# Optimization experiments

Measured on AMD Instinct MI355X. Metric: run time of the kernel, lower is better.

The kernel has to match this reference:

```python
import jax, jax.numpy as jnp
from jax import lax
import numpy as np

B, C, H, W = 64, 3, 224, 224
NPARAM, NSEV, NCHROMA, K = 8, 5, 1, 37
SEVERITY = 3  # ctor default
CHROMA = 0   # random.random()*nchroma made deterministic


def setup_inputs() -> dict:
    key = jax.random.key(0)
    k1, k2, k3, k4, k5 = jax.random.split(key, 5)
    batch = jax.random.uniform(k1, (B, C, H, W), dtype=jnp.float32)
    targets = jax.random.randint(k2, (B,), 0, 1000, dtype=jnp.int32)
    psf_stack = jax.random.uniform(k3, (NPARAM, NSEV, NCHROMA, C, K, K), dtype=jnp.float32)
    params = jax.random.randint(k4, (B,), 0, NPARAM, dtype=jnp.int32)
    weights = jax.random.uniform(k5, (B,), dtype=jnp.float32)
    return {"batch": batch, "targets": targets, "psf_stack": psf_stack,
            "params": params, "weights": weights}


def reference(batch, targets, psf_stack, params, weights):
    # kernels for chosen severity/chroma: [NPARAM, C, K, K]
    kernels = psf_stack[:, SEVERITY - 1, CHROMA]
    k = kernels[params]                      # per-sample kernels [B, C, K, K]
    b, c, h, w = batch.shape
    p = K // 2
    # reflect pad (torch F.pad mode='reflect')
    xp = jnp.pad(batch, ((0, 0), (0, 0), (p, p), (p, p)), mode='reflect')
    # per-sample per-channel (depthwise) conv as one grouped conv with B*C groups
    x = xp.reshape(1, b * c, h + 2 * p, w + 2 * p)
    kw = k.reshape(b * c, 1, K, K)
    blurred = lax.conv_general_dilated(
        x, kw, window_strides=(1, 1), padding='VALID',
        feature_group_count=b * c,
        dimension_numbers=('NCHW', 'OIHW', 'NCHW'),
    ).reshape(b, c, h, w)
    wv = weights.reshape(-1, 1, 1, 1)
    out = (1.0 - wv) * batch + wv * blurred  # normalize is identity by default
    return out, targets
```

## Files before the change

### kernel.cpp

```cpp
#include <hip/hip_runtime.h>

#define BB 64
#define CC 3
#define HH 224
#define WW 224
#define KK 37
#define PP 18
#define PLANE (HH*WW)

#define BM 64
#define BROWS 100
#define BSTR  280
#define FRAGS 2560
#define NTT (8*CC*KK)

typedef __attribute__((ext_vector_type(8)))  __bf16 bf16x8;
typedef __attribute__((ext_vector_type(16))) float  f32x16;

__device__ __forceinline__ unsigned short f2bf(float f) {
    unsigned int u = __float_as_uint(f);
    return (unsigned short)((u + 0x7FFFu + ((u >> 16) & 1u)) >> 16);
}
__device__ __forceinline__ float bf2f(unsigned short h) {
    return __uint_as_float(((unsigned int)h) << 16);
}

__global__ __launch_bounds__(256) void build_frags(
    const float* __restrict__ psf, unsigned short* __restrict__ tt)
{
    const int s = blockIdx.x;
    const int ky = s % KK;
    const int pc = s / KK;
    const int p = pc / CC, c = pc - (pc / CC) * CC;
    const float* wrow = psf + (size_t)(((p*5 + 2)*CC + c)*KK + ky) * KK;
    unsigned short* dst = tt + (size_t)s * FRAGS;
    for (int e = threadIdx.x; e < FRAGS; e += 256) {
        int j = e & 7, ln = (e >> 3) & 31, hi = (e >> 8) & 1, q = e >> 9;
        int kx = 16*q + 8*hi + j - ln;
        dst[e] = (kx >= 0 && kx < KK) ? f2bf(wrow[kx]) : (unsigned short)0;
    }
}

__device__ __forceinline__ void load_bq_ws(bf16x8 (&bq)[5], const unsigned short* kybase) {
    #pragma unroll
    for (int q = 0; q < 5; ++q)
        bq[q] = *(const bf16x8*)(kybase + q*512);
}

__device__ __forceinline__ void load_bq_fb(bf16x8 (&bq)[5], const unsigned short* s_w16,
                                           int ky, int hi, int ln) {
    #pragma unroll
    for (int q = 0; q < 5; ++q) {
        union { bf16x8 v; unsigned short s[8]; } u;
        #pragma unroll
        for (int j = 0; j < 8; ++j) {
            int kx = 16*q + 8*hi + j - ln;
            u.s[j] = (kx >= 0 && kx < KK) ? s_w16[ky*40 + kx] : (unsigned short)0;
        }
        bq[q] = u.v;
    }
}

#define MFMA_(T,Q) T = __builtin_amdgcn_mfma_f32_32x32x16_bf16(af, bq[Q], T, 0, 0, 0)

template<int NT>
__device__ __forceinline__ void compute_ky(const unsigned short* rp, const bf16x8 (&bq)[5],
    f32x16& A0, f32x16& A1, f32x16& A2, f32x16& A3)
{
    bf16x8 af;
#define LDC(c) af = *(const bf16x8*)(rp + 16*(c))
    LDC(0);  MFMA_(A0,0);
    LDC(1);  MFMA_(A0,1);
    LDC(2);  MFMA_(A0,2); MFMA_(A1,0);
    LDC(3);  MFMA_(A0,3); MFMA_(A1,1);
    LDC(4);  MFMA_(A0,4); MFMA_(A1,2); MFMA_(A2,0);
    LDC(5);  MFMA_(A1,3); MFMA_(A2,1);
    if constexpr (NT == 4) {
        LDC(6);  MFMA_(A1,4); MFMA_(A2,2); MFMA_(A3,0);
        LDC(7);  MFMA_(A2,3); MFMA_(A3,1);
        LDC(8);  MFMA_(A2,4); MFMA_(A3,2);
        LDC(9);  MFMA_(A3,3);
        LDC(10); MFMA_(A3,4);
    } else {
        LDC(6);  MFMA_(A1,4); MFMA_(A2,2);
        LDC(7);  MFMA_(A2,3);
        LDC(8);  MFMA_(A2,4);
    }
#undef LDC
}

template<bool FROM_WS, int NT>
__device__ __forceinline__ void kloop(
    const unsigned short* base,
    const unsigned short* fb,
    int hi, int ln,
    f32x16& A0, f32x16& A1, f32x16& A2, f32x16& A3)
{
    bf16x8 bqA[5], bqB[5];
    if constexpr (FROM_WS) load_bq_ws(bqA, fb); else load_bq_fb(bqA, fb, 0, hi, ln);
    for (int ky = 0; ky < KK; ky += 2) {
        if (ky + 1 < KK) {
            if constexpr (FROM_WS) load_bq_ws(bqB, fb + (size_t)(ky + 1)*FRAGS);
            else load_bq_fb(bqB, fb, ky + 1, hi, ln);
        }
        __builtin_amdgcn_s_setprio(1);
        compute_ky<NT>(base + ky*BSTR, bqA, A0, A1, A2, A3);
        __builtin_amdgcn_s_setprio(0);
        if (ky + 1 >= KK) break;
        if (ky + 2 < KK) {
            if constexpr (FROM_WS) load_bq_ws(bqA, fb + (size_t)(ky + 2)*FRAGS);
            else load_bq_fb(bqA, fb, ky + 2, hi, ln);
        }
        __builtin_amdgcn_s_setprio(1);
        compute_ky<NT>(base + (ky + 1)*BSTR, bqB, A0, A1, A2, A3);
        __builtin_amdgcn_s_setprio(0);
    }
}

template<bool FROM_WS>
__global__ __launch_bounds__(256, 2) void optics_mfma(
    const float* __restrict__ batch,
    const float* __restrict__ psf,
    const unsigned short* __restrict__ tt,
    const int* __restrict__ params,
    const float* __restrict__ weights,
    float* __restrict__ out)
{
    __shared__ __align__(16) unsigned short s_band[BROWS*BSTR];
    __shared__ __align__(16) unsigned short s_w16[FROM_WS ? 8 : KK*40];

    const int tid = threadIdx.x;
    const int yband = blockIdx.x;
    const int plane = blockIdx.y;
    const int b = plane / CC, c = plane - b*CC;
    const int y0 = yband * BM;
    const int rows = (HH - y0 < BM) ? (HH - y0) : BM;
    const int brows = rows + KK - 1;
    const int p = params[b];

    const float* src = batch + (size_t)plane * PLANE;
    for (int i = tid; i < brows*56; i += 256) {
        int r = i / 56, g = i - r*56;
        int gy = y0 + r - PP;
        gy = gy < 0 ? -gy : (gy >= HH ? 2*HH - 2 - gy : gy);
        float4 v = *(const float4*)&src[gy*WW + 4*g];
        unsigned int lo  = f2bf(v.x) | ((unsigned int)f2bf(v.y) << 16);
        unsigned int hi2 = f2bf(v.z) | ((unsigned int)f2bf(v.w) << 16);
        unsigned int* d = (unsigned int*)&s_band[r*BSTR + PP + 4*g];
        d[0] = lo; d[1] = hi2;
    }
    for (int i = tid; i < brows*56; i += 256) {
        int r = i / 56, e = i - r*56;
        int col = e < PP ? e : (224 + e);
        int gy = y0 + r - PP;
        gy = gy < 0 ? -gy : (gy >= HH ? 2*HH - 2 - gy : gy);
        int gx = col - PP;
        gx = gx < 0 ? -gx : (gx >= WW ? 2*WW - 2 - gx : gx);
        s_band[r*BSTR + col] = f2bf(src[gy*WW + gx]);
    }
    if constexpr (!FROM_WS) {
        const float* ksrc = psf + (size_t)((p*5 + 2)*CC + c) * (KK*KK);
        for (int i = tid; i < KK*KK; i += 256) {
            int ky_ = i / KK, kx_ = i - ky_*KK;
            s_w16[ky_*40 + kx_] = f2bf(ksrc[i]);
        }
    }
    __syncthreads();

    const int lane = tid & 63;
    const int wid  = tid >> 6;
    const int wr   = wid >> 1;
    const int xh   = wid & 1;
    const int ln   = lane & 31;
    const int hi   = lane >> 5;
    const bool active = (wr == 0) || (rows > 32);

    if (active) {
        const unsigned short* fb;
        if constexpr (FROM_WS)
            fb = tt + (size_t)((p*CC + c)*KK)*FRAGS + hi*256 + ln*8;
        else
            fb = s_w16;
        const unsigned short* base = &s_band[(32*wr + ln)*BSTR + 128*xh + 8*hi];

        f32x16 A0 = {0,0,0,0, 0,0,0,0, 0,0,0,0, 0,0,0,0};
        f32x16 A1 = A0, A2 = A0, A3 = A0;

        if (xh == 0) kloop<FROM_WS, 4>(base, fb, hi, ln, A0, A1, A2, A3);
        else         kloop<FROM_WS, 3>(base, fb, hi, ln, A0, A1, A2, A3);

        const float wt = weights[b];
        const float w1 = 1.0f - wt;
        float* dst = out + (size_t)plane * PLANE;
#define EPI(ACC, GT) { \
        _Pragma("unroll") \
        for (int r = 0; r < 16; ++r) { \
            const int rowL = (r & 3) + 8*(r >> 2) + 4*hi; \
            const int yo = y0 + 32*wr + rowL; \
            const int xo = 32*(GT) + ln; \
            const float orig = bf2f(s_band[(32*wr + rowL + PP)*BSTR + xo + PP]); \
            dst[yo*WW + xo] = w1*orig + wt*ACC[r]; \
        } }
        if (xh == 0) { EPI(A0, 0) EPI(A1, 1) EPI(A2, 2) EPI(A3, 3) }
        else         { EPI(A0, 4) EPI(A1, 5) EPI(A2, 6) }
#undef EPI
    }
}

__global__ void copy_targets(const int* __restrict__ t, float* __restrict__ out) {
    int i = threadIdx.x;
    if (i < BB) out[i] = (float)t[i];
}

extern "C" void kernel_launch(void* const* d_in, const int* in_sizes, int n_in,
                              void* d_out, int out_size, void* d_ws, size_t ws_size,
                              hipStream_t stream) {
    const float* batch   = (const float*)d_in[0];
    const int*   targets = (const int*)d_in[1];
    const float* psf     = (const float*)d_in[2];
    const int*   params  = (const int*)d_in[3];
    const float* weights = (const float*)d_in[4];
    float* out = (float*)d_out;
    unsigned short* tt = (unsigned short*)d_ws;

    const size_t need = (size_t)NTT * FRAGS * sizeof(unsigned short);
    dim3 grid((HH + BM - 1) / BM, BB*CC);

    if (ws_size >= need) {
        build_frags<<<NTT, 256, 0, stream>>>(psf, tt);
        optics_mfma<true><<<grid, 256, 0, stream>>>(batch, psf, tt, params, weights, out);
    } else {
        optics_mfma<false><<<grid, 256, 0, stream>>>(batch, psf, tt, params, weights, out);
    }
    copy_targets<<<1, 64, 0, stream>>>(targets, out + (size_t)BB*CC*PLANE);
}
```

Before: 79.91 us.

## Shrink row band to 32 rows and remap warps to column tiles

The row band per block drops from 64 to 32 output rows, so every band is full (7 bands per plane) and the idle-warp case on the last band goes away. The four waves now each cover two 32-column tiles (the last wave one) instead of a 2x2 split, with fewer accumulators per wave and launch bounds raised for higher occupancy. The cost is more halo overhead per output row (68 band rows for 32 outputs versus 100 for 64), plus more weight-fragment reloads and more blocks. The LDS row stride shrinks to 264 and the padding columns past the image are zero-filled.

```diff
diff --git a/kernel.cpp b/kernel.cpp
--- a/kernel.cpp
+++ b/kernel.cpp
@@ -8,9 +8,9 @@
 #define PP 18
 #define PLANE (HH*WW)
 
-#define BM 64
-#define BROWS 100
-#define BSTR  280
+#define BM 32
+#define BROWS 68
+#define BSTR 264
 #define FRAGS 2560
 #define NTT (8*CC*KK)
 
@@ -65,26 +65,24 @@
 
 template<int NT>
 __device__ __forceinline__ void compute_ky(const unsigned short* rp, const bf16x8 (&bq)[5],
-    f32x16& A0, f32x16& A1, f32x16& A2, f32x16& A3)
+                                           f32x16& A0, f32x16& A1)
 {
     bf16x8 af;
 #define LDC(c) af = *(const bf16x8*)(rp + 16*(c))
-    LDC(0);  MFMA_(A0,0);
-    LDC(1);  MFMA_(A0,1);
-    LDC(2);  MFMA_(A0,2); MFMA_(A1,0);
-    LDC(3);  MFMA_(A0,3); MFMA_(A1,1);
-    LDC(4);  MFMA_(A0,4); MFMA_(A1,2); MFMA_(A2,0);
-    LDC(5);  MFMA_(A1,3); MFMA_(A2,1);
-    if constexpr (NT == 4) {
-        LDC(6);  MFMA_(A1,4); MFMA_(A2,2); MFMA_(A3,0);
-        LDC(7);  MFMA_(A2,3); MFMA_(A3,1);
-        LDC(8);  MFMA_(A2,4); MFMA_(A3,2);
-        LDC(9);  MFMA_(A3,3);
-        LDC(10); MFMA_(A3,4);
+    if constexpr (NT == 2) {
+        LDC(0); MFMA_(A0,0);
+        LDC(1); MFMA_(A0,1);
+        LDC(2); MFMA_(A0,2); MFMA_(A1,0);
+        LDC(3); MFMA_(A0,3); MFMA_(A1,1);
+        LDC(4); MFMA_(A0,4); MFMA_(A1,2);
+        LDC(5); MFMA_(A1,3);
+        LDC(6); MFMA_(A1,4);
     } else {
-        LDC(6);  MFMA_(A1,4); MFMA_(A2,2);
-        LDC(7);  MFMA_(A2,3);
-        LDC(8);  MFMA_(A2,4);
+        LDC(0); MFMA_(A0,0);
+        LDC(1); MFMA_(A0,1);
+        LDC(2); MFMA_(A0,2);
+        LDC(3); MFMA_(A0,3);
+        LDC(4); MFMA_(A0,4);
     }
 #undef LDC
 }
@@ -93,8 +91,7 @@
 __device__ __forceinline__ void kloop(
     const unsigned short* base,
     const unsigned short* fb,
-    int hi, int ln,
-    f32x16& A0, f32x16& A1, f32x16& A2, f32x16& A3)
+    int hi, int ln, f32x16& A0, f32x16& A1)
 {
     bf16x8 bqA[5], bqB[5];
     if constexpr (FROM_WS) load_bq_ws(bqA, fb); else load_bq_fb(bqA, fb, 0, hi, ln);
@@ -104,7 +101,7 @@
             else load_bq_fb(bqB, fb, ky + 1, hi, ln);
         }
         __builtin_amdgcn_s_setprio(1);
-        compute_ky<NT>(base + ky*BSTR, bqA, A0, A1, A2, A3);
+        compute_ky<NT>(base + ky*BSTR, bqA, A0, A1);
         __builtin_amdgcn_s_setprio(0);
         if (ky + 1 >= KK) break;
         if (ky + 2 < KK) {
@@ -112,13 +109,13 @@
             else load_bq_fb(bqA, fb, ky + 2, hi, ln);
         }
         __builtin_amdgcn_s_setprio(1);
-        compute_ky<NT>(base + (ky + 1)*BSTR, bqB, A0, A1, A2, A3);
+        compute_ky<NT>(base + (ky + 1)*BSTR, bqB, A0, A1);
         __builtin_amdgcn_s_setprio(0);
     }
 }
 
 template<bool FROM_WS>
-__global__ __launch_bounds__(256, 2) void optics_mfma(
+__global__ __launch_bounds__(256, 4) void optics_mfma(
     const float* __restrict__ batch,
     const float* __restrict__ psf,
     const unsigned short* __restrict__ tt,
@@ -126,7 +123,7 @@
     const float* __restrict__ weights,
     float* __restrict__ out)
 {
-    __shared__ __align__(16) unsigned short s_band[BROWS*BSTR];
+    __shared__ __align__(16) unsigned short s_band[BROWS*BSTR + 16];
     __shared__ __align__(16) unsigned short s_w16[FROM_WS ? 8 : KK*40];
 
     const int tid = threadIdx.x;
@@ -134,12 +131,10 @@
     const int plane = blockIdx.y;
     const int b = plane / CC, c = plane - b*CC;
     const int y0 = yband * BM;
-    const int rows = (HH - y0 < BM) ? (HH - y0) : BM;
-    const int brows = rows + KK - 1;
     const int p = params[b];
 
     const float* src = batch + (size_t)plane * PLANE;
-    for (int i = tid; i < brows*56; i += 256) {
+    for (int i = tid; i < BROWS*56; i += 256) {
         int r = i / 56, g = i - r*56;
         int gy = y0 + r - PP;
         gy = gy < 0 ? -gy : (gy >= HH ? 2*HH - 2 - gy : gy);
@@ -149,15 +144,20 @@
         unsigned int* d = (unsigned int*)&s_band[r*BSTR + PP + 4*g];
         d[0] = lo; d[1] = hi2;
     }
-    for (int i = tid; i < brows*56; i += 256) {
-        int r = i / 56, e = i - r*56;
+    for (int i = tid; i < BROWS*40; i += 256) {
+        int r = i / 40, e = i - r*40;
         int col = e < PP ? e : (224 + e);
-        int gy = y0 + r - PP;
-        gy = gy < 0 ? -gy : (gy >= HH ? 2*HH - 2 - gy : gy);
-        int gx = col - PP;
-        gx = gx < 0 ? -gx : (gx >= WW ? 2*WW - 2 - gx : gx);
-        s_band[r*BSTR + col] = f2bf(src[gy*WW + gx]);
-    }
+        unsigned short v = 0;
+        if (col < 260) {
+            int gy = y0 + r - PP;
+            gy = gy < 0 ? -gy : (gy >= HH ? 2*HH - 2 - gy : gy);
+            int gx = col - PP;
+            gx = gx < 0 ? -gx : (gx >= WW ? 2*WW - 2 - gx : gx);
+            v = f2bf(src[gy*WW + gx]);
+        }
+        s_band[r*BSTR + col] = v;
+    }
+    if (tid < 16) s_band[BROWS*BSTR + tid] = 0;
     if constexpr (!FROM_WS) {
         const float* ksrc = psf + (size_t)((p*5 + 2)*CC + c) * (KK*KK);
         for (int i = tid; i < KK*KK; i += 256) {
@@ -168,43 +168,38 @@
     __syncthreads();
 
     const int lane = tid & 63;
-    const int wid  = tid >> 6;
-    const int wr   = wid >> 1;
-    const int xh   = wid & 1;
+    const int w    = tid >> 6;
     const int ln   = lane & 31;
     const int hi   = lane >> 5;
-    const bool active = (wr == 0) || (rows > 32);
-
-    if (active) {
-        const unsigned short* fb;
-        if constexpr (FROM_WS)
-            fb = tt + (size_t)((p*CC + c)*KK)*FRAGS + hi*256 + ln*8;
-        else
-            fb = s_w16;
-        const unsigned short* base = &s_band[(32*wr + ln)*BSTR + 128*xh + 8*hi];
-
-        f32x16 A0 = {0,0,0,0, 0,0,0,0, 0,0,0,0, 0,0,0,0};
-        f32x16 A1 = A0, A2 = A0, A3 = A0;
-
-        if (xh == 0) kloop<FROM_WS, 4>(base, fb, hi, ln, A0, A1, A2, A3);
-        else         kloop<FROM_WS, 3>(base, fb, hi, ln, A0, A1, A2, A3);
-
-        const float wt = weights[b];
-        const float w1 = 1.0f - wt;
-        float* dst = out + (size_t)plane * PLANE;
+
+    const unsigned short* fb;
+    if constexpr (FROM_WS)
+        fb = tt + (size_t)((p*CC + c)*KK)*FRAGS + hi*256 + ln*8;
+    else
+        fb = s_w16;
+    const unsigned short* base = &s_band[ln*BSTR + 64*w + 8*hi];
+
+    f32x16 A0 = {0,0,0,0, 0,0,0,0, 0,0,0,0, 0,0,0,0};
+    f32x16 A1 = A0;
+
+    if (w < 3) kloop<FROM_WS, 2>(base, fb, hi, ln, A0, A1);
+    else       kloop<FROM_WS, 1>(base, fb, hi, ln, A0, A1);
+
+    const float wt = weights[b];
+    const float w1 = 1.0f - wt;
+    float* dst = out + (size_t)plane * PLANE;
 #define EPI(ACC, GT) { \
-        _Pragma("unroll") \
-        for (int r = 0; r < 16; ++r) { \
-            const int rowL = (r & 3) + 8*(r >> 2) + 4*hi; \
-            const int yo = y0 + 32*wr + rowL; \
-            const int xo = 32*(GT) + ln; \
-            const float orig = bf2f(s_band[(32*wr + rowL + PP)*BSTR + xo + PP]); \
-            dst[yo*WW + xo] = w1*orig + wt*ACC[r]; \
-        } }
-        if (xh == 0) { EPI(A0, 0) EPI(A1, 1) EPI(A2, 2) EPI(A3, 3) }
-        else         { EPI(A0, 4) EPI(A1, 5) EPI(A2, 6) }
+    _Pragma("unroll") \
+    for (int r = 0; r < 16; ++r) { \
+        const int rowL = (r & 3) + 8*(r >> 2) + 4*hi; \
+        const int yo = y0 + rowL; \
+        const int xo = 32*(GT) + ln; \
+        const float orig = bf2f(s_band[(rowL + PP)*BSTR + xo + PP]); \
+        dst[yo*WW + xo] = w1*orig + wt*ACC[r]; \
+    } }
+    EPI(A0, 2*w)
+    if (w < 3) EPI(A1, 2*w + 1)
 #undef EPI
-    }
 }
 
 __global__ void copy_targets(const int* __restrict__ t, float* __restrict__ out) {
@@ -224,7 +219,7 @@
     unsigned short* tt = (unsigned short*)d_ws;
 
     const size_t need = (size_t)NTT * FRAGS * sizeof(unsigned short);
-    dim3 grid((HH + BM - 1) / BM, BB*CC);
+    dim3 grid(HH / BM, BB*CC);
 
     if (ws_size >= need) {
         build_frags<<<NTT, 256, 0, stream>>>(psf, tt);
```

Measured after the change: 80.22 us. No clear change (+0.4%).

## Prefetch A fragments per ky row, shrink LDS stride, raise occupancy, fuse target copy

Applied to the files above, without the earlier changes.

The inner loop now loads all A-operand fragments for the next kernel row into a register array before issuing MFMAs, double-buffering them alongside the B fragments so LDS reads overlap compute. The band row stride shrinks from 280 to 264 so the LDS footprint allows three blocks per CU, and launch bounds are raised to 3. The target copy moves into build_frags to drop a kernel launch. The risks are higher register pressure from two 11-entry fragment arrays under a tighter register budget, and possible bank-conflict changes from the new stride.

```diff
diff --git a/kernel.cpp b/kernel.cpp
--- a/kernel.cpp
+++ b/kernel.cpp
@@ -10,9 +10,10 @@
 
 #define BM 64
 #define BROWS 100
-#define BSTR  280
+#define BSTR 264
 #define FRAGS 2560
 #define NTT (8*CC*KK)
+#define TT_BYTES ((size_t)NTT * FRAGS * sizeof(unsigned short))
 
 typedef __attribute__((ext_vector_type(8)))  __bf16 bf16x8;
 typedef __attribute__((ext_vector_type(16))) float  f32x16;
@@ -26,7 +27,8 @@
 }
 
 __global__ __launch_bounds__(256) void build_frags(
-    const float* __restrict__ psf, unsigned short* __restrict__ tt)
+    const float* __restrict__ psf, unsigned short* __restrict__ tt,
+    const int* __restrict__ targets, float* __restrict__ tout)
 {
     const int s = blockIdx.x;
     const int ky = s % KK;
@@ -39,6 +41,7 @@
         int kx = 16*q + 8*hi + j - ln;
         dst[e] = (kx >= 0 && kx < KK) ? f2bf(wrow[kx]) : (unsigned short)0;
     }
+    if (s == 0 && threadIdx.x < BB) tout[threadIdx.x] = (float)targets[threadIdx.x];
 }
 
 __device__ __forceinline__ void load_bq_ws(bf16x8 (&bq)[5], const unsigned short* kybase) {
@@ -61,33 +64,32 @@
     }
 }
 
-#define MFMA_(T,Q) T = __builtin_amdgcn_mfma_f32_32x32x16_bf16(af, bq[Q], T, 0, 0, 0)
+template<int NC>
+__device__ __forceinline__ void load_af(bf16x8 (&af)[11], const unsigned short* rp) {
+    #pragma unroll
+    for (int c = 0; c < NC; ++c)
+        af[c] = *(const bf16x8*)(rp + 16*c);
+}
+
+#define MFMA4(T,AF,Q) T = __builtin_amdgcn_mfma_f32_32x32x16_bf16(af[AF], bq[Q], T, 0, 0, 0)
 
 template<int NT>
-__device__ __forceinline__ void compute_ky(const unsigned short* rp, const bf16x8 (&bq)[5],
-    f32x16& A0, f32x16& A1, f32x16& A2, f32x16& A3)
-{
-    bf16x8 af;
-#define LDC(c) af = *(const bf16x8*)(rp + 16*(c))
-    LDC(0);  MFMA_(A0,0);
-    LDC(1);  MFMA_(A0,1);
-    LDC(2);  MFMA_(A0,2); MFMA_(A1,0);
-    LDC(3);  MFMA_(A0,3); MFMA_(A1,1);
-    LDC(4);  MFMA_(A0,4); MFMA_(A1,2); MFMA_(A2,0);
-    LDC(5);  MFMA_(A1,3); MFMA_(A2,1);
-    if constexpr (NT == 4) {
-        LDC(6);  MFMA_(A1,4); MFMA_(A2,2); MFMA_(A3,0);
-        LDC(7);  MFMA_(A2,3); MFMA_(A3,1);
-        LDC(8);  MFMA_(A2,4); MFMA_(A3,2);
-        LDC(9);  MFMA_(A3,3);
-        LDC(10); MFMA_(A3,4);
-    } else {
-        LDC(6);  MFMA_(A1,4); MFMA_(A2,2);
-        LDC(7);  MFMA_(A2,3);
-        LDC(8);  MFMA_(A2,4);
-    }
-#undef LDC
-}
+__device__ __forceinline__ void compute_ky(const bf16x8 (&af)[11], const bf16x8 (&bq)[5],
+                                           f32x16& A0, f32x16& A1, f32x16& A2, f32x16& A3)
+{
+    MFMA4(A0,0,0);
+    MFMA4(A0,1,1);
+    MFMA4(A0,2,2); MFMA4(A1,2,0);
+    MFMA4(A0,3,3); MFMA4(A1,3,1);
+    MFMA4(A0,4,4); MFMA4(A1,4,2); MFMA4(A2,4,0);
+    MFMA4(A1,5,3); MFMA4(A2,5,1);
+    MFMA4(A1,6,4); MFMA4(A2,6,2); if constexpr (NT == 4) { MFMA4(A3,6,0); }
+    MFMA4(A2,7,3); if constexpr (NT == 4) { MFMA4(A3,7,1); }
+    MFMA4(A2,8,4); if constexpr (NT == 4) { MFMA4(A3,8,2); MFMA4(A3,9,3); MFMA4(A3,10,4); }
+}
+
+#define SP1 __builtin_amdgcn_s_setprio(1)
+#define SP0 __builtin_amdgcn_s_setprio(0)
 
 template<bool FROM_WS, int NT>
 __device__ __forceinline__ void kloop(
@@ -96,29 +98,29 @@
     int hi, int ln,
     f32x16& A0, f32x16& A1, f32x16& A2, f32x16& A3)
 {
-    bf16x8 bqA[5], bqB[5];
+    constexpr int NC = (NT == 4) ? 11 : 9;
+    bf16x8 afA[11], afB[11], bqA[5], bqB[5];
+    load_af<NC>(afA, base);
     if constexpr (FROM_WS) load_bq_ws(bqA, fb); else load_bq_fb(bqA, fb, 0, hi, ln);
     for (int ky = 0; ky < KK; ky += 2) {
         if (ky + 1 < KK) {
+            load_af<NC>(afB, base + (ky + 1)*BSTR);
             if constexpr (FROM_WS) load_bq_ws(bqB, fb + (size_t)(ky + 1)*FRAGS);
             else load_bq_fb(bqB, fb, ky + 1, hi, ln);
         }
-        __builtin_amdgcn_s_setprio(1);
-        compute_ky<NT>(base + ky*BSTR, bqA, A0, A1, A2, A3);
-        __builtin_amdgcn_s_setprio(0);
+        SP1; compute_ky<NT>(afA, bqA, A0, A1, A2, A3); SP0;
         if (ky + 1 >= KK) break;
         if (ky + 2 < KK) {
+            load_af<NC>(afA, base + (ky + 2)*BSTR);
             if constexpr (FROM_WS) load_bq_ws(bqA, fb + (size_t)(ky + 2)*FRAGS);
             else load_bq_fb(bqA, fb, ky + 2, hi, ln);
         }
-        __builtin_amdgcn_s_setprio(1);
-        compute_ky<NT>(base + (ky + 1)*BSTR, bqB, A0, A1, A2, A3);
-        __builtin_amdgcn_s_setprio(0);
+        SP1; compute_ky<NT>(afB, bqB, A0, A1, A2, A3); SP0;
     }
 }
 
 template<bool FROM_WS>
-__global__ __launch_bounds__(256, 2) void optics_mfma(
+__global__ __launch_bounds__(256, 3) void optics_mfma(
     const float* __restrict__ batch,
     const float* __restrict__ psf,
     const unsigned short* __restrict__ tt,
@@ -126,7 +128,7 @@
     const float* __restrict__ weights,
     float* __restrict__ out)
 {
-    __shared__ __align__(16) unsigned short s_band[BROWS*BSTR];
+    __shared__ __align__(16) unsigned short s_band[BROWS*BSTR + 16];
     __shared__ __align__(16) unsigned short s_w16[FROM_WS ? 8 : KK*40];
 
     const int tid = threadIdx.x;
@@ -149,15 +151,20 @@
         unsigned int* d = (unsigned int*)&s_band[r*BSTR + PP + 4*g];
         d[0] = lo; d[1] = hi2;
     }
-    for (int i = tid; i < brows*56; i += 256) {
-        int r = i / 56, e = i - r*56;
+    for (int i = tid; i < brows*40; i += 256) {
+        int r = i / 40, e = i - r*40;
         int col = e < PP ? e : (224 + e);
-        int gy = y0 + r - PP;
-        gy = gy < 0 ? -gy : (gy >= HH ? 2*HH - 2 - gy : gy);
-        int gx = col - PP;
-        gx = gx < 0 ? -gx : (gx >= WW ? 2*WW - 2 - gx : gx);
-        s_band[r*BSTR + col] = f2bf(src[gy*WW + gx]);
-    }
+        unsigned short v = 0;
+        if (col < 260) {
+            int gy = y0 + r - PP;
+            gy = gy < 0 ? -gy : (gy >= HH ? 2*HH - 2 - gy : gy);
+            int gx = col - PP;
+            gx = gx < 0 ? -gx : (gx >= WW ? 2*WW - 2 - gx : gx);
+            v = f2bf(src[gy*WW + gx]);
+        }
+        s_band[r*BSTR + col] = v;
+    }
+    if (tid < 16) s_band[brows*BSTR + tid] = 0;
     if constexpr (!FROM_WS) {
         const float* ksrc = psf + (size_t)((p*5 + 2)*CC + c) * (KK*KK);
         for (int i = tid; i < KK*KK; i += 256) {
@@ -223,14 +230,14 @@
     float* out = (float*)d_out;
     unsigned short* tt = (unsigned short*)d_ws;
 
-    const size_t need = (size_t)NTT * FRAGS * sizeof(unsigned short);
     dim3 grid((HH + BM - 1) / BM, BB*CC);
 
-    if (ws_size >= need) {
-        build_frags<<<NTT, 256, 0, stream>>>(psf, tt);
+    if (ws_size >= TT_BYTES) {
+        build_frags<<<NTT, 256, 0, stream>>>(psf, tt, targets,
+                                             out + (size_t)BB*CC*PLANE);
         optics_mfma<true><<<grid, 256, 0, stream>>>(batch, psf, tt, params, weights, out);
     } else {
         optics_mfma<false><<<grid, 256, 0, stream>>>(batch, psf, tt, params, weights, out);
-    }
-    copy_targets<<<1, 64, 0, stream>>>(targets, out + (size_t)BB*CC*PLANE);
-}
+        copy_targets<<<1, 64, 0, stream>>>(targets, out + (size_t)BB*CC*PLANE);
+    }
+}
```

Measured after the change: 127.9 us. 60.0% more time.
